# Kernel tuning notes

Measured on AMD Instinct MI355X. Metric: run time of the kernel, lower is better.

Reference implementation:

```python
import jax, jax.numpy as jnp
import numpy as np

D_MODEL = 2048
NUM_HEADS = 16
THETA = 10000.0


def setup_inputs() -> dict:
    key = jax.random.key(0)
    ks = jax.random.split(key, 5)
    bs, S, d = 4, 2048, D_MODEL
    std = (2.0 / (d + d)) ** 0.5
    x = jax.random.normal(ks[0], (bs, S, d), dtype=jnp.float32)
    wq = jax.random.normal(ks[1], (d, d), dtype=jnp.float32) * std
    wk = jax.random.normal(ks[2], (d, d), dtype=jnp.float32) * std
    wv = jax.random.normal(ks[3], (d, d), dtype=jnp.float32) * std
    wo = jax.random.normal(ks[4], (d, d), dtype=jnp.float32) * std
    return {"x": x, "wq": wq, "wk": wk, "wv": wv, "wo": wo}


def _rope(t, cos, sin):
    # t: (bs, H, S, d_k); cos/sin: (S, d_k) interleaved-duplicated
    # rotate_half: (-x1, x0, -x3, x2, ...)
    x_even = t[..., 0::2]
    x_odd = t[..., 1::2]
    rot = jnp.stack((-x_odd, x_even), axis=-1).reshape(t.shape)
    return t * cos + rot * sin


def reference(x, wq, wk, wv, wo):
    bs, S, d = x.shape
    H = NUM_HEADS
    dk = d // H
    # QKV projections (Linear has no bias; weight stored (out, in), applied as x @ W.T)
    q = (x @ wq.T).reshape(bs, S, H, dk).transpose(0, 2, 1, 3)  # (bs,H,S,dk)
    k = (x @ wk.T).reshape(bs, S, H, dk).transpose(0, 2, 1, 3)
    v = (x @ wv.T).reshape(bs, S, H, dk).transpose(0, 2, 1, 3)

    # RoPE tables (interleaved convention)
    half = dk // 2
    inv_freq = THETA ** (-2.0 * jnp.arange(half, dtype=jnp.float32) / dk)  # (half,)
    pos = jnp.arange(S, dtype=jnp.float32)
    ang = pos[:, None] * inv_freq[None, :]  # (S, half)
    cos = jnp.repeat(jnp.cos(ang), 2, axis=-1)  # (S, dk), (c0,c0,c1,c1,...)
    sin = jnp.repeat(jnp.sin(ang), 2, axis=-1)
    q = _rope(q, cos, sin)
    k = _rope(k, cos, sin)

    scale = 1.0 / jnp.sqrt(jnp.asarray(dk, dtype=x.dtype))
    attn = jnp.einsum("bhqd,bhkd->bhqk", q, k) * scale  # (bs,H,S,S)
    causal = jnp.tril(jnp.ones((S, S), dtype=bool))
    attn = jnp.where(causal, attn, -jnp.inf)
    probs = jax.nn.softmax(attn, axis=-1)
    out = jnp.einsum("bhqk,bhkd->bhqd", probs, v)  # (bs,H,S,dk)
    out = out.transpose(0, 2, 1, 3).reshape(bs, S, d)
    return out @ wo.T
```

## Files before the change

### kernel.cpp

```cpp
#include <hip/hip_runtime.h>
#include <hip/hip_bf16.h>
#include <cstdint>
#include <cstddef>

typedef unsigned short u16;
typedef unsigned int u32;
typedef __attribute__((ext_vector_type(8))) short short8;
typedef __attribute__((ext_vector_type(4))) short bfx4;
typedef __attribute__((ext_vector_type(4))) float f32x4;

#define D_MODEL 2048
#define SEQ     2048
#define BATCH   4
#define NHEADS  16
#define DKH     128
#define NTOK    (BATCH*SEQ)

typedef const __attribute__((address_space(1))) void* gptr_t;
typedef __attribute__((address_space(3))) void* lptr_t;

__device__ inline float bf2f(u16 u) {
  union { float f; u32 i; } x; x.i = ((u32)u) << 16; return x.f;
}
__device__ inline u16 f2bf(float f) {
  union { float f; u32 i; } x; x.f = f;
  return (u16)((x.i + 0x7FFFu + ((x.i >> 16) & 1u)) >> 16);
}
__device__ inline u32 packbf2(float a, float b) {
  union { float f; u32 i; } xa, xb; xa.f = a; xb.f = b;
  return (xa.i >> 16) | (xb.i & 0xFFFF0000u);
}

__global__ void cvt_kernel(const float* __restrict__ in, u16* __restrict__ out, int n8) {
  int i = blockIdx.x * 256 + threadIdx.x;
  if (i >= n8) return;
  const float* p = in + (size_t)i * 8;
  short8 v;
#pragma unroll
  for (int j = 0; j < 8; ++j) v[j] = (short)f2bf(p[j]);
  *(short8*)(out + (size_t)i * 8) = v;
}

__global__ void cvtw_kernel(const float* __restrict__ wq, const float* __restrict__ wk,
                            const float* __restrict__ wv, const float* __restrict__ wo,
                            u16* __restrict__ wall) {
  int by = blockIdx.y;
  const float* src = by == 0 ? wq : by == 1 ? wk : by == 2 ? wv : wo;
  int i = blockIdx.x * 256 + threadIdx.x;
  const float* p = src + (size_t)i * 8;
  short8 v;
#pragma unroll
  for (int j = 0; j < 8; ++j) v[j] = (short)f2bf(p[j]);
  *(short8*)(wall + (size_t)by * D_MODEL * D_MODEL + (size_t)i * 8) = v;
}

__global__ void trig_kernel(float* __restrict__ cosT, float* __restrict__ sinT) {
  int i = blockIdx.x * 256 + threadIdx.x;
  int s = i >> 6, j = i & 63;
  float inv = powf(10000.0f, -2.0f * (float)j / 128.0f);
  float ang = (float)s * inv;
  cosT[i] = cosf(ang);
  sinT[i] = sinf(ang);
}

template<int F32OUT>
__global__ __launch_bounds__(512, 2)
void gemm_bt256(const u16* __restrict__ A, const u16* __restrict__ B,
                void* __restrict__ Cv, int M, int N, int K) {
  __shared__ u16 lds[2][2][256 * 64];
  const int T = threadIdx.x;
  const int lane = T & 63, w = T >> 6;
  const int lo = lane & 15, hi = lane >> 4;
  const int wr = w >> 2, wc = w & 3;
  const int id = blockIdx.x;
  const int bm = (id >> 3) * 256, bn = (id & 7) * 256;
  const int nt = K >> 6;

  const int qrow_base = (w & 3) * 8 + (w >> 2) * 128;
  const int lrow = lane >> 3;
  const int lchunk = lane & 7;

  auto STAGEQ = [&](int buf, int z, int kt) {
    int r0 = z * 32 + qrow_base;
    int rn = r0 + lrow;
    int ck = lchunk ^ (rn & 7);
    __builtin_amdgcn_global_load_lds(
        (gptr_t)(A + (size_t)(bm + rn) * K + kt * 64 + ck * 8),
        (lptr_t)(&lds[buf][0][0] + r0 * 64), 16, 0, 0);
    __builtin_amdgcn_global_load_lds(
        (gptr_t)(B + (size_t)(bn + rn) * K + kt * 64 + ck * 8),
        (lptr_t)(&lds[buf][1][0] + r0 * 64), 16, 0, 0);
  };

  f32x4 acc[8][4] = {};
  short8 bfrag[4][2];

#define GPHASE(qq, tt, cc) do {                                                \
    short8 af[2][2];                                                           \
    _Pragma("unroll")                                                          \
    for (int m2 = 0; m2 < 2; ++m2) {                                           \
      int row = wr * 128 + (2 * (qq) + m2) * 16 + lo;                          \
      _Pragma("unroll")                                                        \
      for (int c = 0; c < 2; ++c)                                              \
        af[m2][c] = *(const short8*)((const char*)&lds[cc][0][0] +             \
            (row << 7) + ((c * 64 + hi * 16) ^ ((row & 7) << 4)));             \
    }                                                                          \
    if ((qq) == 0) {                                                           \
      _Pragma("unroll")                                                        \
      for (int ni = 0; ni < 4; ++ni) {                                         \
        int row = wc * 64 + ni * 16 + lo;                                      \
        _Pragma("unroll")                                                      \
        for (int c = 0; c < 2; ++c)                                            \
          bfrag[ni][c] = *(const short8*)((const char*)&lds[cc][1][0] +        \
              (row << 7) + ((c * 64 + hi * 16) ^ ((row & 7) << 4)));           \
      }                                                                        \
    }                                                                          \
    { int zz = ((qq) + 3) & 3;                                                 \
      int stt = (qq) == 0 ? (tt) + 1 : (tt) + 2;                               \
      int sbuf = (qq) == 0 ? ((tt) + 1) & 1 : (tt) & 1;                        \
      if (stt < nt) STAGEQ(sbuf, zz, stt); }                                   \
    __builtin_amdgcn_s_barrier();                                              \
    asm volatile("s_waitcnt lgkmcnt(0)" ::: "memory");                         \
    __builtin_amdgcn_sched_barrier(0);                                         \
    __builtin_amdgcn_s_setprio(1);                                             \
    _Pragma("unroll")                                                          \
    for (int m2 = 0; m2 < 2; ++m2)                                             \
      _Pragma("unroll")                                                        \
      for (int ni = 0; ni < 4; ++ni)                                           \
        _Pragma("unroll")                                                      \
        for (int c = 0; c < 2; ++c)                                            \
          acc[2 * (qq) + m2][ni] = __builtin_amdgcn_mfma_f32_16x16x32_bf16(    \
              af[m2][c], bfrag[ni][c], acc[2 * (qq) + m2][ni], 0, 0, 0);       \
    __builtin_amdgcn_s_setprio(0);                                             \
    __builtin_amdgcn_sched_barrier(0);                                         \
    __builtin_amdgcn_s_barrier();                                              \
  } while (0)

#pragma unroll
  for (int z = 0; z < 4; ++z) STAGEQ(0, z, 0);
#pragma unroll
  for (int z = 0; z < 3; ++z) STAGEQ(1, z, 1);
  asm volatile("s_waitcnt vmcnt(6)" ::: "memory");
  __builtin_amdgcn_s_barrier();

  for (int t = 0; t < nt; ++t) {
    const int cur = t & 1;
    GPHASE(0, t, cur);
    GPHASE(1, t, cur);
    GPHASE(2, t, cur);
    GPHASE(3, t, cur);
    if (t == nt - 2) asm volatile("s_waitcnt vmcnt(0)" ::: "memory");
    else             asm volatile("s_waitcnt vmcnt(6)" ::: "memory");
    __builtin_amdgcn_s_barrier();
  }
#undef GPHASE

#pragma unroll
  for (int mi = 0; mi < 8; ++mi)
#pragma unroll
    for (int ni = 0; ni < 4; ++ni) {
      int row = bm + wr * 128 + mi * 16 + hi * 4;
      int col = bn + wc * 64 + ni * 16 + lo;
#pragma unroll
      for (int r = 0; r < 4; ++r) {
        if (F32OUT)
          ((float*)Cv)[(size_t)(row + r) * N + col] = acc[mi][ni][r];
        else
          ((u16*)Cv)[(size_t)(row + r) * N + col] = f2bf(acc[mi][ni][r]);
      }
    }
}

__global__ void rope_kernel(u16* __restrict__ t, const float* __restrict__ cosT,
                            const float* __restrict__ sinT, float premul) {
  int i = blockIdx.x * 256 + threadIdx.x;
  int row = i >> 8;
  int g = i & 255;
  int s = row & (SEQ - 1);
  int col = g << 3;
  int j0 = (col & 127) >> 1;
  short8 v = *(short8*)(t + (size_t)row * D_MODEL + col);
#pragma unroll
  for (int p = 0; p < 4; ++p) {
    float c  = cosT[s * 64 + j0 + p];
    float sn = sinT[s * 64 + j0 + p];
    float e = bf2f((u16)v[2 * p]), o = bf2f((u16)v[2 * p + 1]);
    v[2 * p]     = (short)f2bf((e * c - o * sn) * premul);
    v[2 * p + 1] = (short)f2bf((o * c + e * sn) * premul);
  }
  *(short8*)(t + (size_t)row * D_MODEL + col) = v;
}

__global__ void vt_kernel(const u16* __restrict__ V, u16* __restrict__ VT) {
  __shared__ u16 tbuf[64][66];
  int bh = blockIdx.z;
  int b = bh >> 4, h = bh & 15;
  int s0 = blockIdx.x << 6, d0 = blockIdx.y << 6;
  for (int i = threadIdx.x; i < 512; i += 256) {
    int sr = i >> 3, c8 = (i & 7) << 3;
    short8 v = *(const short8*)(V + (size_t)(b * SEQ + s0 + sr) * D_MODEL + h * DKH + d0 + c8);
#pragma unroll
    for (int j = 0; j < 8; ++j) tbuf[sr][c8 + j] = (u16)v[j];
  }
  __syncthreads();
  for (int i = threadIdx.x; i < 512; i += 256) {
    int dr = i >> 3, s8 = (i & 7) << 3;
    short8 v;
#pragma unroll
    for (int j = 0; j < 8; ++j) v[j] = (short)tbuf[s8 + j][dr];
    *(short8*)(VT + ((size_t)bh * DKH + d0 + dr) * SEQ + s0 + s8) = v;
  }
}

__device__ __forceinline__ void attn_band(
    int band, int b, int h, int bh,
    const u16* __restrict__ Q, const u16* __restrict__ K,
    const u16* __restrict__ VT, u16* __restrict__ O,
    const float* __restrict__ cosT, const float* __restrict__ sinT,
    u16 (*Ksb)[64 * 128], u16 (*Vsb)[128 * 64], u16* Pw)
{
  const int T = threadIdx.x, lane = T & 63, w = T >> 6;
  const int lo = lane & 15, hi = lane >> 4;
  const int qrow0 = band * 128 + w * 16 + lo;
  const int qrow1 = qrow0 + 64;
  const int qt0 = band * 2;
  const int ktmax = band * 2 + 1;
  const int swzC = (lo & 7) << 4;
  const float SC = 0.08838834764831845f * 1.4426950408889634f;

  short8 qf0[4], qf1[4];
#pragma unroll
  for (int t2 = 0; t2 < 2; ++t2) {
    int qrow = t2 ? qrow1 : qrow0;
    const u16* Qp = Q + (size_t)(b * SEQ + qrow) * D_MODEL + h * DKH;
    const float* cp = cosT + qrow * 64;
    const float* sp = sinT + qrow * 64;
#pragma unroll
    for (int c = 0; c < 4; ++c) {
      short8 v = *(const short8*)(Qp + c * 32 + hi * 8);
#pragma unroll
      for (int p = 0; p < 4; ++p) {
        float cc = cp[c * 16 + hi * 4 + p] * SC;
        float sn = sp[c * 16 + hi * 4 + p] * SC;
        float e = bf2f((u16)v[2 * p]), o = bf2f((u16)v[2 * p + 1]);
        v[2 * p]     = (short)f2bf(e * cc - o * sn);
        v[2 * p + 1] = (short)f2bf(o * cc + e * sn);
      }
      if (t2) qf1[c] = v; else qf0[c] = v;
    }
  }

  f32x4 ot0[8] = {}, ot1[8] = {};
  float m0 = -1e30f, l0 = 0.f, m1 = -1e30f, l1 = 0.f;

  const u16* Kbase = K + ((size_t)b * SEQ) * D_MODEL + h * DKH;
  const u16* Vbase = VT + (size_t)bh * DKH * SEQ;

  auto STAGE = [&](int buf, int kt2) {
    const int kb2 = kt2 << 6;
#pragma unroll
    for (int q = 0; q < 4; ++q) {
      int base = q * 256 + (T & 192);
      int s = base + lane;
      int kv = s >> 4, ck = (s & 15) ^ (kv & 7);
      __builtin_amdgcn_global_load_lds(
          (gptr_t)(Kbase + (size_t)(kb2 + kv) * D_MODEL + ck * 8),
          (lptr_t)(Ksb[buf] + (size_t)base * 8), 16, 0, 0);
      int d = s >> 3, cv2 = (s & 7) ^ (d & 7);
      __builtin_amdgcn_global_load_lds(
          (gptr_t)(Vbase + (size_t)d * SEQ + kb2 + cv2 * 8),
          (lptr_t)(Vsb[buf] + (size_t)base * 8), 16, 0, 0);
    }
  };

  STAGE(0, 0);
  __syncthreads();
  int cur = 0;

  for (int kt = 0; kt <= ktmax; ++kt) {
    if (kt < ktmax) STAGE(cur ^ 1, kt + 1);
    const int kb = kt << 6;
    const u16* Ks = Ksb[cur];
    const u16* Vs = Vsb[cur];

    f32x4 sa0[4], sa1[4];
    __builtin_amdgcn_s_setprio(1);
#pragma unroll
    for (int g = 0; g < 4; ++g) {
      f32x4 s40 = {0.f, 0.f, 0.f, 0.f}, s41 = {0.f, 0.f, 0.f, 0.f};
      int krow = g * 16 + lo;
#pragma unroll
      for (int c = 0; c < 4; ++c) {
        int o = ((krow << 8) + c * 64 + hi * 16) ^ ((krow & 7) << 4);
        short8 kf = *(const short8*)((const char*)Ks + o);
        s40 = __builtin_amdgcn_mfma_f32_16x16x32_bf16(kf, qf0[c], s40, 0, 0, 0);
        s41 = __builtin_amdgcn_mfma_f32_16x16x32_bf16(kf, qf1[c], s41, 0, 0, 0);
      }
      sa0[g] = s40; sa1[g] = s41;
    }
    __builtin_amdgcn_s_setprio(0);

    const bool dg0 = (kt >= qt0), dg1 = (kt == ktmax);
    float pm0 = -1e30f, pm1 = -1e30f;
#pragma unroll
    for (int g = 0; g < 4; ++g)
#pragma unroll
      for (int r = 0; r < 4; ++r) {
        int kvg = kb + g * 16 + hi * 4 + r;
        float sv0 = sa0[g][r], sv1 = sa1[g][r];
        if (dg0 && kvg > qrow0) sv0 = -1e30f;
        if (dg1 && kvg > qrow1) sv1 = -1e30f;
        sa0[g][r] = sv0; sa1[g][r] = sv1;
        pm0 = fmaxf(pm0, sv0); pm1 = fmaxf(pm1, sv1);
      }
    pm0 = fmaxf(pm0, __shfl_xor(pm0, 16));
    pm0 = fmaxf(pm0, __shfl_xor(pm0, 32));
    pm1 = fmaxf(pm1, __shfl_xor(pm1, 16));
    pm1 = fmaxf(pm1, __shfl_xor(pm1, 32));

    if (!__all((pm0 <= m0 + 8.0f) & (pm1 <= m1 + 8.0f))) {
      float mn0 = fmaxf(m0, pm0), mn1 = fmaxf(m1, pm1);
      float sc0 = __builtin_amdgcn_exp2f(m0 - mn0);
      float sc1 = __builtin_amdgcn_exp2f(m1 - mn1);
      l0 *= sc0; l1 *= sc1;
#pragma unroll
      for (int g2 = 0; g2 < 8; ++g2)
#pragma unroll
        for (int r = 0; r < 4; ++r) { ot0[g2][r] *= sc0; ot1[g2][r] *= sc1; }
      m0 = mn0; m1 = mn1;
    }

    float rs0 = 0.f, rs1 = 0.f;
#pragma unroll
    for (int g = 0; g < 4; ++g) {
      float a0 = __builtin_amdgcn_exp2f(sa0[g][0] - m0);
      float a1 = __builtin_amdgcn_exp2f(sa0[g][1] - m0);
      float a2 = __builtin_amdgcn_exp2f(sa0[g][2] - m0);
      float a3 = __builtin_amdgcn_exp2f(sa0[g][3] - m0);
      float b0 = __builtin_amdgcn_exp2f(sa1[g][0] - m1);
      float b1 = __builtin_amdgcn_exp2f(sa1[g][1] - m1);
      float b2 = __builtin_amdgcn_exp2f(sa1[g][2] - m1);
      float b3 = __builtin_amdgcn_exp2f(sa1[g][3] - m1);
      rs0 += (a0 + a1) + (a2 + a3);
      rs1 += (b0 + b1) + (b2 + b3);
      int off = lo * 128 + ((g * 32 + hi * 8) ^ swzC);
      *(u32*)((char*)Pw + off)            = packbf2(a0, a1);
      *(u32*)((char*)Pw + off + 4)        = packbf2(a2, a3);
      *(u32*)((char*)Pw + 2048 + off)     = packbf2(b0, b1);
      *(u32*)((char*)Pw + 2048 + off + 4) = packbf2(b2, b3);
    }
    rs0 += __shfl_xor(rs0, 16); rs0 += __shfl_xor(rs0, 32);
    rs1 += __shfl_xor(rs1, 16); rs1 += __shfl_xor(rs1, 32);
    l0 += rs0; l1 += rs1;

    __builtin_amdgcn_s_setprio(1);
#pragma unroll
    for (int c2 = 0; c2 < 2; ++c2) {
      int pb = lo * 128 + ((c2 * 64 + hi * 16) ^ swzC);
      short8 pf0 = *(const short8*)((char*)Pw + pb);
      short8 pf1 = *(const short8*)((char*)Pw + 2048 + pb);
#pragma unroll
      for (int g2 = 0; g2 < 8; ++g2) {
        int vrow = g2 * 16 + lo;
        int vo = ((vrow << 7) + c2 * 64 + hi * 16) ^ ((vrow & 7) << 4);
        short8 vf = *(const short8*)((const char*)Vs + vo);
        ot0[g2] = __builtin_amdgcn_mfma_f32_16x16x32_bf16(vf, pf0, ot0[g2], 0, 0, 0);
        ot1[g2] = __builtin_amdgcn_mfma_f32_16x16x32_bf16(vf, pf1, ot1[g2], 0, 0, 0);
      }
    }
    __builtin_amdgcn_s_setprio(0);

    __syncthreads();
    cur ^= 1;
  }

  float il0 = 1.0f / l0, il1 = 1.0f / l1;
  u16* Op0 = O + (size_t)(b * SEQ + qrow0) * D_MODEL + h * DKH + hi * 4;
  u16* Op1 = O + (size_t)(b * SEQ + qrow1) * D_MODEL + h * DKH + hi * 4;
#pragma unroll
  for (int g2 = 0; g2 < 8; ++g2) {
    bfx4 v0, v1;
#pragma unroll
    for (int r = 0; r < 4; ++r) {
      v0[r] = (short)f2bf(ot0[g2][r] * il0);
      v1[r] = (short)f2bf(ot1[g2][r] * il1);
    }
    *(bfx4*)(Op0 + g2 * 16) = v0;
    *(bfx4*)(Op1 + g2 * 16) = v1;
  }
}

__global__ __launch_bounds__(256)
void attn_kernel(const u16* __restrict__ Q, const u16* __restrict__ K,
                 const u16* __restrict__ VT, u16* __restrict__ O,
                 const float* __restrict__ cosT, const float* __restrict__ sinT) {
  __shared__ u16 Ksb[2][64 * 128];
  __shared__ u16 Vsb[2][128 * 64];
  __shared__ u16 Ps[4 * 2048];
  const int wg = blockIdx.x;
  const int xcd = wg & 7, idx = wg >> 3;
  const int bh = xcd * 8 + (idx >> 3);
  const int tp = idx & 7;
  const int b = bh >> 4, h = bh & 15;
  u16* Pw = Ps + (threadIdx.x >> 6) * 2048;
  attn_band(15 - tp, b, h, bh, Q, K, VT, O, cosT, sinT, Ksb, Vsb, Pw);
  attn_band(tp,      b, h, bh, Q, K, VT, O, cosT, sinT, Ksb, Vsb, Pw);
}

extern "C" void kernel_launch(void* const* d_in, const int* in_sizes, int n_in,
                              void* d_out, int out_size, void* d_ws, size_t ws_size,
                              hipStream_t stream) {
  const float* x  = (const float*)d_in[0];
  const float* wq = (const float*)d_in[1];
  const float* wk = (const float*)d_in[2];
  const float* wv = (const float*)d_in[3];
  const float* wo = (const float*)d_in[4];
  float* out = (float*)d_out;

  const size_t TOKB = (size_t)NTOK * D_MODEL * 2;
  const size_t WB   = (size_t)D_MODEL * D_MODEL * 2;
  char* p = (char*)d_ws;
  u16* xb  = (u16*)p; p += TOKB;
  u16* wqb = (u16*)p; p += WB;
  u16* wkb = (u16*)p; p += WB;
  u16* wvb = (u16*)p; p += WB;
  u16* wob = (u16*)p; p += WB;
  u16* Qb  = (u16*)p; p += TOKB;
  u16* Kb  = (u16*)p; p += TOKB;
  u16* Vb  = (u16*)p; p += TOKB;
  u16* VTb = (u16*)p; p += TOKB;
  u16* Ob  = (u16*)p; p += TOKB;
  float* cosT = (float*)p; p += (size_t)SEQ * 64 * 4;
  float* sinT = (float*)p; p += (size_t)SEQ * 64 * 4;

  cvt_kernel<<<8192, 256, 0, stream>>>(x, xb, 2097152);
  cvtw_kernel<<<dim3(2048, 4), 256, 0, stream>>>(wq, wk, wv, wo, wqb);
  trig_kernel<<<512, 256, 0, stream>>>(cosT, sinT);

  gemm_bt256<0><<<256, 512, 0, stream>>>(xb, wqb, Qb, NTOK, D_MODEL, D_MODEL);
  gemm_bt256<0><<<256, 512, 0, stream>>>(xb, wkb, Kb, NTOK, D_MODEL, D_MODEL);
  gemm_bt256<0><<<256, 512, 0, stream>>>(xb, wvb, Vb, NTOK, D_MODEL, D_MODEL);

  rope_kernel<<<8192, 256, 0, stream>>>(Kb, cosT, sinT, 1.0f);

  vt_kernel<<<dim3(32, 2, 64), 256, 0, stream>>>(Vb, VTb);

  attn_kernel<<<512, 256, 0, stream>>>(Qb, Kb, VTb, Ob, cosT, sinT);

  gemm_bt256<1><<<256, 512, 0, stream>>>(Ob, wob, out, NTOK, D_MODEL, D_MODEL);
}
```

Measured before the change: 513.8 us.

## Stage V tiles through registers into single LDS buffer instead of double-buffered async loads

V tiles are now prefetched into registers with ordinary global loads during compute and written to a single shared-memory V buffer after the PV matmul. K keeps its double-buffered async global-to-LDS path. This roughly halves V's LDS footprint, which may allow more resident workgroups. The cost is an extra barrier per iteration, more VGPR pressure, and V writes to LDS that are exposed rather than overlapped.

```diff
diff --git a/kernel.cpp b/kernel.cpp
--- a/kernel.cpp
+++ b/kernel.cpp
@@ -217,7 +217,7 @@
     const u16* __restrict__ Q, const u16* __restrict__ K,
     const u16* __restrict__ VT, u16* __restrict__ O,
     const float* __restrict__ cosT, const float* __restrict__ sinT,
-    u16 (*Ksb)[64 * 128], u16 (*Vsb)[128 * 64], u16* Pw)
+    u16 (*Ksb)[64 * 128], u16* Vs, u16* Pw)
 {
   const int T = threadIdx.x, lane = T & 63, w = T >> 6;
   const int lo = lane & 15, hi = lane >> 4;
@@ -256,7 +256,7 @@
   const u16* Kbase = K + ((size_t)b * SEQ) * D_MODEL + h * DKH;
   const u16* Vbase = VT + (size_t)bh * DKH * SEQ;
 
-  auto STAGE = [&](int buf, int kt2) {
+  auto STAGE_K = [&](int buf, int kt2) {
     const int kb2 = kt2 << 6;
 #pragma unroll
     for (int q = 0; q < 4; ++q) {
@@ -266,22 +266,44 @@
       __builtin_amdgcn_global_load_lds(
           (gptr_t)(Kbase + (size_t)(kb2 + kv) * D_MODEL + ck * 8),
           (lptr_t)(Ksb[buf] + (size_t)base * 8), 16, 0, 0);
-      int d = s >> 3, cv2 = (s & 7) ^ (d & 7);
-      __builtin_amdgcn_global_load_lds(
-          (gptr_t)(Vbase + (size_t)d * SEQ + kb2 + cv2 * 8),
-          (lptr_t)(Vsb[buf] + (size_t)base * 8), 16, 0, 0);
     }
   };
 
-  STAGE(0, 0);
+  short8 vreg[4];
+  auto VREGLOAD = [&](int kt2) {
+    const int kb2 = kt2 << 6;
+#pragma unroll
+    for (int q = 0; q < 4; ++q) {
+      int s = q * 256 + T;
+      int d = s >> 3, cv = s & 7;
+      vreg[q] = *(const short8*)(Vbase + (size_t)d * SEQ + kb2 + cv * 8);
+    }
+  };
+  auto VWRITE = [&](int unused) {
+    (void)unused;
+#pragma unroll
+    for (int q = 0; q < 4; ++q) {
+      int s = q * 256 + T;
+      int d = s >> 3, cv = s & 7;
+      int off = (d << 7) + ((cv << 4) ^ ((d & 7) << 4));
+      *(short8*)((char*)Vs + off) = vreg[q];
+    }
+  };
+
+  __syncthreads();
+  VREGLOAD(0);
+  STAGE_K(0, 0);
+  VWRITE(0);
   __syncthreads();
   int cur = 0;
 
   for (int kt = 0; kt <= ktmax; ++kt) {
-    if (kt < ktmax) STAGE(cur ^ 1, kt + 1);
+    if (kt < ktmax) {
+      STAGE_K(cur ^ 1, kt + 1);
+      VREGLOAD(kt + 1);
+    }
     const int kb = kt << 6;
     const u16* Ks = Ksb[cur];
-    const u16* Vs = Vsb[cur];
 
     f32x4 sa0[4], sa1[4];
     __builtin_amdgcn_s_setprio(1);
@@ -370,7 +392,11 @@
     }
     __builtin_amdgcn_s_setprio(0);
 
-    __syncthreads();
+    if (kt < ktmax) {
+      __syncthreads();
+      VWRITE(kt + 1);
+      __syncthreads();
+    }
     cur ^= 1;
   }
 
@@ -395,7 +421,7 @@
                  const u16* __restrict__ VT, u16* __restrict__ O,
                  const float* __restrict__ cosT, const float* __restrict__ sinT) {
   __shared__ u16 Ksb[2][64 * 128];
-  __shared__ u16 Vsb[2][128 * 64];
+  __shared__ u16 Vs[128 * 64];
   __shared__ u16 Ps[4 * 2048];
   const int wg = blockIdx.x;
   const int xcd = wg & 7, idx = wg >> 3;
@@ -403,8 +429,8 @@
   const int tp = idx & 7;
   const int b = bh >> 4, h = bh & 15;
   u16* Pw = Ps + (threadIdx.x >> 6) * 2048;
-  attn_band(15 - tp, b, h, bh, Q, K, VT, O, cosT, sinT, Ksb, Vsb, Pw);
-  attn_band(tp,      b, h, bh, Q, K, VT, O, cosT, sinT, Ksb, Vsb, Pw);
+  attn_band(15 - tp, b, h, bh, Q, K, VT, O, cosT, sinT, Ksb, Vs, Pw);
+  attn_band(tp,      b, h, bh, Q, K, VT, O, cosT, sinT, Ksb, Vs, Pw);
 }
 
 extern "C" void kernel_launch(void* const* d_in, const int* in_sizes, int n_in,
```

New measurement: 541.4 us. 5.4% more time.
